# Performance work log

Measured on AMD Instinct MI355X. Metric: run time of the kernel, lower is better.

Reference implementation:

```python
import jax, jax.numpy as jnp
import numpy as np

B, N, M = 8, 4096, 77
Q_DIM, CTX_DIM = 1024, 768
H, D = 16, 64
INNER = H * D  # 1024


def setup_inputs() -> dict:
    key = jax.random.key(0)
    ks = jax.random.split(key, 7)
    x = jax.random.normal(ks[0], (B, N, Q_DIM), dtype=jnp.float32)
    context = jax.random.normal(ks[1], (B, M, CTX_DIM), dtype=jnp.float32)
    # Linear weights stored as [in, out] so y = x @ W (no bias for q/k/v).
    Wq = jax.random.normal(ks[2], (Q_DIM, INNER), dtype=jnp.float32) * (Q_DIM ** -0.5)
    Wk = jax.random.normal(ks[3], (CTX_DIM, INNER), dtype=jnp.float32) * (CTX_DIM ** -0.5)
    Wv = jax.random.normal(ks[4], (CTX_DIM, INNER), dtype=jnp.float32) * (CTX_DIM ** -0.5)
    Wo = jax.random.normal(ks[5], (INNER, Q_DIM), dtype=jnp.float32) * (INNER ** -0.5)
    bo = jax.random.normal(ks[6], (Q_DIM,), dtype=jnp.float32) * 0.01
    return {"x": x, "context": context, "Wq": Wq, "Wk": Wk, "Wv": Wv, "Wo": Wo, "bo": bo}


def reference(x, context, Wq, Wk, Wv, Wo, bo):
    scale = D ** -0.5
    # Project and split heads: [B, S, H*D] -> [B, H, S, D]
    def heads(t):
        b, s, _ = t.shape
        return t.reshape(b, s, H, D).transpose(0, 2, 1, 3)
    q = heads(x @ Wq)        # [B, H, N, D]
    k = heads(context @ Wk)  # [B, H, M, D]
    v = heads(context @ Wv)  # [B, H, M, D]
    scores = jnp.einsum('bhid,bhjd->bhij', q, k) * scale  # [B, H, N, M]
    attn = jax.nn.softmax(scores, axis=-1)
    out = jnp.einsum('bhij,bhjd->bhid', attn, v)          # [B, H, N, D]
    out = out.transpose(0, 2, 1, 3).reshape(x.shape[0], x.shape[1], INNER)
    return out @ Wo + bo  # dropout p=0.0 -> identity
```

## Files before the change

### kernel.cpp

```cpp
#include <hip/hip_runtime.h>
#include <hip/hip_bf16.h>

typedef _Float16 f16x8 __attribute__((ext_vector_type(8)));
typedef float f32x4 __attribute__((ext_vector_type(4)));

#define MFMA16(a, b, c) __builtin_amdgcn_mfma_f32_16x16x32_f16(a, b, c, 0, 0, 0)

__device__ __forceinline__ void load_lds16(const void* g, void* l) {
  __builtin_amdgcn_global_load_lds(
      (__attribute__((address_space(1))) void*)g,
      (__attribute__((address_space(3))) void*)l, 16, 0, 0);
}

__global__ __launch_bounds__(256) void k_cvt16(const float* __restrict__ in,
                                               _Float16* __restrict__ out, int n8) {
  int stride = gridDim.x * blockDim.x;
  for (int i = blockIdx.x * blockDim.x + threadIdx.x; i < n8; i += stride) {
    const float4* p = (const float4*)(in + (size_t)i * 8);
    float4 a = p[0], b = p[1];
    f16x8 v = {(_Float16)a.x, (_Float16)a.y, (_Float16)a.z, (_Float16)a.w,
               (_Float16)b.x, (_Float16)b.y, (_Float16)b.z, (_Float16)b.w};
    *(f16x8*)(out + (size_t)i * 8) = v;
  }
}

__global__ __launch_bounds__(256) void k_transpose(const float* __restrict__ in,
                                                   _Float16* __restrict__ out, int K, int N) {
  __shared__ float tile[64][65];
  int k0 = blockIdx.y * 64, n0 = blockIdx.x * 64;
  int t = threadIdx.x;
  {
    int nn = t & 63, kb = t >> 6;
#pragma unroll
    for (int i = 0; i < 16; ++i) {
      int kk = kb + i * 4;
      tile[kk][nn] = in[(size_t)(k0 + kk) * N + n0 + nn];
    }
  }
  __syncthreads();
  {
    int kk = t & 63, nb = t >> 6;
#pragma unroll
    for (int i = 0; i < 16; ++i) {
      int nn = nb + i * 4;
      out[(size_t)(n0 + nn) * K + k0 + kk] = (_Float16)tile[kk][nn];
    }
  }
}

__global__ __launch_bounds__(64) void k_kvproj(const _Float16* __restrict__ ctxh,
                                               const _Float16* __restrict__ Wkt,
                                               const _Float16* __restrict__ Wvt,
                                               _Float16* __restrict__ Kg,
                                               _Float16* __restrict__ Vtg) {
  int mt = blockIdx.x, nt = blockIdx.y;
  int lane = threadIdx.x;
  int l15 = lane & 15, lhi = lane >> 4;
  int arow = mt * 16 + l15;
  if (arow > 615) arow = 615;
  const _Float16* ap = ctxh + (size_t)arow * 768 + lhi * 8;
  const _Float16* kp = Wkt + (size_t)(nt * 16 + l15) * 768 + lhi * 8;
  const _Float16* vp = Wvt + (size_t)(nt * 16 + l15) * 768 + lhi * 8;
  f32x4 ak = {0.f, 0.f, 0.f, 0.f}, av = {0.f, 0.f, 0.f, 0.f};
#pragma unroll 4
  for (int ks = 0; ks < 24; ++ks) {
    f16x8 a = *(const f16x8*)(ap + ks * 32);
    f16x8 bk = *(const f16x8*)(kp + ks * 32);
    f16x8 bv = *(const f16x8*)(vp + ks * 32);
    ak = MFMA16(a, bk, ak);
    av = MFMA16(a, bv, av);
  }
  int n = nt * 16 + l15, h = n >> 6, d = n & 63;
#pragma unroll
  for (int j = 0; j < 4; ++j) {
    int gm = mt * 16 + lhi * 4 + j;
    if (gm < 616) {
      int b = gm / 77, m = gm - b * 77;
      Kg[((size_t)(b * 16 + h) * 77 + m) * 64 + d] = (_Float16)ak[j];
      Vtg[((size_t)(b * 16 + h) * 64 + d) * 128 + m] = (_Float16)av[j];
    }
  }
}

__global__ __launch_bounds__(256) void k_attn(const _Float16* __restrict__ Qh,
                                              const _Float16* __restrict__ Kg,
                                              const _Float16* __restrict__ Vtg,
                                              _Float16* __restrict__ Out) {
  __shared__ __align__(16) char Kl[80 * 128];
  __shared__ __align__(16) char Vl[64 * 256];
  __shared__ __align__(16) char Pl[4 * 16 * 256];
  int bh = blockIdx.y, b = bh >> 4, h = bh & 15;
  int t = threadIdx.x, wid = t >> 6, lane = t & 63;
  int l15 = lane & 15, lhi = lane >> 4;

  const _Float16* Kgp = Kg + (size_t)bh * (77 * 64);
  const _Float16* Vgp = Vtg + (size_t)bh * (64 * 128);

  for (int idx = t; idx < 640; idx += 256) {
    int m = idx >> 3, c = (idx & 7) * 8;
    f16x8 v = {};
    if (m < 77) v = *(const f16x8*)(Kgp + m * 64 + c);
    *(f16x8*)(Kl + ((m * 128 + c * 2) ^ ((m & 7) << 4))) = v;
  }
  for (int idx = t; idx < 1024; idx += 256) {
    int d = idx >> 4, c = (idx & 15) * 8;
    f16x8 v = *(const f16x8*)(Vgp + d * 128 + c);
    *(f16x8*)(Vl + ((d * 256 + c * 2) ^ ((d & 7) << 4))) = v;
  }
  char* myP = Pl + wid * 4096;
#pragma unroll
  for (int i = 0; i < 4; ++i) *(f16x8*)(myP + lane * 64 + i * 16) = f16x8{};
  __syncthreads();

  int qrow = b * 4096 + blockIdx.x * 64 + wid * 16 + l15;
  const _Float16* qp = Qh + (size_t)qrow * 1024 + h * 64 + lhi * 8;
  f16x8 q0 = *(const f16x8*)qp;
  f16x8 q1 = *(const f16x8*)(qp + 32);

  float e[5][4];
  float mx[4] = {-1e30f, -1e30f, -1e30f, -1e30f};
#pragma unroll
  for (int ct = 0; ct < 5; ++ct) {
    int m = ct * 16 + l15;
    int d0b = lhi * 16;
    f16x8 k0 = *(const f16x8*)(Kl + ((m * 128 + d0b) ^ ((m & 7) << 4)));
    f16x8 k1 = *(const f16x8*)(Kl + ((m * 128 + 64 + d0b) ^ ((m & 7) << 4)));
    f32x4 acc = {0.f, 0.f, 0.f, 0.f};
    acc = MFMA16(q0, k0, acc);
    acc = MFMA16(q1, k1, acc);
    bool valid = m < 77;
#pragma unroll
    for (int j = 0; j < 4; ++j) {
      float v = valid ? acc[j] * 0.125f : -1e30f;
      e[ct][j] = v;
      mx[j] = fmaxf(mx[j], v);
    }
  }
#pragma unroll
  for (int off = 1; off < 16; off <<= 1)
#pragma unroll
    for (int j = 0; j < 4; ++j) mx[j] = fmaxf(mx[j], __shfl_xor(mx[j], off, 64));
  float sm[4] = {0.f, 0.f, 0.f, 0.f};
#pragma unroll
  for (int ct = 0; ct < 5; ++ct)
#pragma unroll
    for (int j = 0; j < 4; ++j) {
      float ev = __expf(e[ct][j] - mx[j]);
      e[ct][j] = ev;
      sm[j] += ev;
    }
#pragma unroll
  for (int off = 1; off < 16; off <<= 1)
#pragma unroll
    for (int j = 0; j < 4; ++j) sm[j] += __shfl_xor(sm[j], off, 64);
  float rs[4];
#pragma unroll
  for (int j = 0; j < 4; ++j) rs[j] = 1.0f / sm[j];

#pragma unroll
  for (int ct = 0; ct < 5; ++ct) {
    int m = ct * 16 + l15;
#pragma unroll
    for (int j = 0; j < 4; ++j) {
      int r = lhi * 4 + j;
      *(_Float16*)(myP + ((r * 256 + m * 2) ^ ((r & 7) << 4))) =
          (_Float16)(e[ct][j] * rs[j]);
    }
  }

  f32x4 o[4] = {{0.f,0.f,0.f,0.f},{0.f,0.f,0.f,0.f},{0.f,0.f,0.f,0.f},{0.f,0.f,0.f,0.f}};
#pragma unroll
  for (int ks = 0; ks < 3; ++ks) {
    int m0b = ks * 64 + lhi * 16;
    f16x8 pa = *(const f16x8*)(myP + ((l15 * 256 + m0b) ^ ((l15 & 7) << 4)));
#pragma unroll
    for (int dt = 0; dt < 4; ++dt) {
      int d = dt * 16 + l15;
      f16x8 vb = *(const f16x8*)(Vl + ((d * 256 + m0b) ^ ((d & 7) << 4)));
      o[dt] = MFMA16(pa, vb, o[dt]);
    }
  }
  _Float16* op = Out + (size_t)(b * 4096 + blockIdx.x * 64 + wid * 16) * 1024 + h * 64;
#pragma unroll
  for (int dt = 0; dt < 4; ++dt)
#pragma unroll
    for (int j = 0; j < 4; ++j) {
      int r = lhi * 4 + j;
      op[(size_t)r * 1024 + dt * 16 + l15] = (_Float16)o[dt][j];
    }
}

template <int FINAL>
__global__ __launch_bounds__(512, 2) void k_gemm3(const _Float16* __restrict__ A,
                                                  const _Float16* __restrict__ Bt,
                                                  void* __restrict__ Cout,
                                                  const float* __restrict__ bias,
                                                  int M, int N, int K) {
  __shared__ __align__(16) char lds[131072];
  const int t = threadIdx.x, wid = t >> 6, lane = t & 63;
  const int wr = wid >> 2, wc = wid & 3;
  const int l15 = lane & 15, lhi = lane >> 4;

  int nwg = gridDim.x, bid = blockIdx.x;
  int wg = ((nwg & 7) == 0) ? ((bid & 7) * (nwg >> 3) + (bid >> 3)) : bid;
  const int nTN = N >> 8;
  const int tm = wg / nTN, tn = wg % nTN;

  const _Float16* Ag = A + (size_t)tm * 256 * K;
  const _Float16* Bg = Bt + (size_t)tn * 256 * K;
  const size_t stg = (size_t)(wid * 8 + (lane >> 3)) * K +
                     (size_t)(((lane & 7) ^ (((lane >> 5) & 1) << 1)) * 8);
  const int dstg = wid * 1024;

  const int xb = ((l15 >> 2) & 1) << 1;
  const int aoff = wr * 16384 + l15 * 128 + ((lhi ^ xb) << 4);
  const int boff = 32768 + wc * 8192 + l15 * 128 + ((lhi ^ xb) << 4);

  f32x4 acc[8][4];
#pragma unroll
  for (int i = 0; i < 8; ++i)
#pragma unroll
    for (int j = 0; j < 4; ++j) acc[i][j] = f32x4{0.f, 0.f, 0.f, 0.f};
  f16x8 a[4][2], b0[2][2], b1[2][2];

#define STG_A(T, RB) load_lds16(Ag + stg + (size_t)(RB) * K + (T) * 64, \
                                lds + ((T) & 1) * 65536 + (RB) * 128 + dstg)
#define STG_B(T, RB) load_lds16(Bg + stg + (size_t)(RB) * K + (T) * 64, \
                                lds + ((T) & 1) * 65536 + 32768 + (RB) * 128 + dstg)
#define RD_A(BUF, MH) { const char* p_ = lds + (BUF) * 65536 + aoff + (MH) * 8192;  \
    _Pragma("unroll") for (int mf = 0; mf < 4; ++mf)                                \
      _Pragma("unroll") for (int kk = 0; kk < 2; ++kk)                              \
        a[mf][kk] = *(const f16x8*)(p_ + mf * 2048 + kk * 64); }
#define RD_B(BUF, NH, BREG) { const char* q_ = lds + (BUF) * 65536 + boff + (NH) * 4096; \
    _Pragma("unroll") for (int nf = 0; nf < 2; ++nf)                                \
      _Pragma("unroll") for (int kk = 0; kk < 2; ++kk)                              \
        BREG[nf][kk] = *(const f16x8*)(q_ + nf * 2048 + kk * 64); }
#define MM(MH, NH, BREG) { __builtin_amdgcn_s_setprio(1);                           \
    _Pragma("unroll") for (int mf = 0; mf < 4; ++mf)                                \
      _Pragma("unroll") for (int nf = 0; nf < 2; ++nf)                              \
        _Pragma("unroll") for (int kk = 0; kk < 2; ++kk)                            \
          acc[(MH)*4+mf][(NH)*2+nf] = MFMA16(a[mf][kk], BREG[nf][kk],               \
                                             acc[(MH)*4+mf][(NH)*2+nf]);            \
    __builtin_amdgcn_s_setprio(0); }
#define VM6 asm volatile("s_waitcnt vmcnt(6)" ::: "memory")
#define VM0 asm volatile("s_waitcnt vmcnt(0)" ::: "memory")
#define BAR __builtin_amdgcn_s_barrier()

  const int nT = K >> 6;

  STG_A(0, 0); STG_A(0, 64); STG_A(0, 128); STG_A(0, 192);
  STG_B(0, 0); STG_B(0, 64); STG_B(0, 128); STG_B(0, 192);
  STG_A(1, 0); STG_A(1, 128);
  STG_B(1, 0); STG_B(1, 64); STG_B(1, 128); STG_B(1, 192);
  asm volatile("s_waitcnt vmcnt(6)" ::: "memory");
  BAR;

  const int nPair = (nT - 2) >> 1;
  for (int i = 0; i < nPair; ++i) {
    const int t0 = 2 * i;
    RD_B(0, 0, b0); RD_A(0, 0); STG_A(t0 + 1, 64); STG_A(t0 + 1, 192); BAR; MM(0, 0, b0); BAR;
    RD_B(0, 1, b1); STG_A(t0 + 2, 0); STG_A(t0 + 2, 128); BAR; MM(0, 1, b1); BAR;
    RD_A(0, 1); STG_B(t0 + 2, 0); STG_B(t0 + 2, 64); BAR; MM(1, 1, b1); BAR;
    STG_B(t0 + 2, 128); STG_B(t0 + 2, 192); VM6; BAR; MM(1, 0, b0); BAR;
    RD_B(1, 0, b0); RD_A(1, 0); STG_A(t0 + 2, 64); STG_A(t0 + 2, 192); BAR; MM(0, 0, b0); BAR;
    RD_B(1, 1, b1); STG_A(t0 + 3, 0); STG_A(t0 + 3, 128); BAR; MM(0, 1, b1); BAR;
    RD_A(1, 1); STG_B(t0 + 3, 0); STG_B(t0 + 3, 64); BAR; MM(1, 1, b1); BAR;
    STG_B(t0 + 3, 128); STG_B(t0 + 3, 192); VM6; BAR; MM(1, 0, b0); BAR;
  }
  RD_B(0, 0, b0); RD_A(0, 0); STG_A(nT - 1, 64); STG_A(nT - 1, 192); BAR; MM(0, 0, b0); BAR;
  RD_B(0, 1, b1); BAR; MM(0, 1, b1); BAR;
  RD_A(0, 1); BAR; MM(1, 1, b1); BAR;
  VM0; BAR; MM(1, 0, b0); BAR;
  RD_B(1, 0, b0); RD_A(1, 0); BAR; MM(0, 0, b0); BAR;
  RD_B(1, 1, b1); BAR; MM(0, 1, b1); BAR;
  RD_A(1, 1); BAR; MM(1, 1, b1); BAR;
  MM(1, 0, b0);

  const long rbase = (long)tm * 256 + wr * 128;
  const int cbase = tn * 256 + wc * 64;
#pragma unroll
  for (int mf = 0; mf < 8; ++mf)
#pragma unroll
    for (int nf = 0; nf < 4; ++nf) {
      int c = cbase + nf * 16 + l15;
      float bv = FINAL ? bias[c] : 0.f;
#pragma unroll
      for (int j = 0; j < 4; ++j) {
        long r = rbase + mf * 16 + lhi * 4 + j;
        float v = acc[mf][nf][j];
        if (FINAL) ((float*)Cout)[r * N + c] = v + bv;
        else ((_Float16*)Cout)[r * N + c] = (_Float16)v;
      }
    }
#undef STG_A
#undef STG_B
#undef RD_A
#undef RD_B
#undef MM
#undef VM6
#undef VM0
#undef BAR
}

extern "C" void kernel_launch(void* const* d_in, const int* in_sizes, int n_in,
                              void* d_out, int out_size, void* d_ws, size_t ws_size,
                              hipStream_t stream) {
  const float* x   = (const float*)d_in[0];
  const float* ctx = (const float*)d_in[1];
  const float* Wq  = (const float*)d_in[2];
  const float* Wk  = (const float*)d_in[3];
  const float* Wv  = (const float*)d_in[4];
  const float* Wo  = (const float*)d_in[5];
  const float* bo  = (const float*)d_in[6];

  char* ws = (char*)d_ws;
  _Float16* xh   = (_Float16*)(ws + 0);
  _Float16* Wqt  = (_Float16*)(ws + 67108864);
  _Float16* Wkt  = (_Float16*)(ws + 69206016);
  _Float16* Wvt  = (_Float16*)(ws + 70778880);
  _Float16* Wot  = (_Float16*)(ws + 72351744);
  _Float16* ctxh = (_Float16*)(ws + 74448896);
  _Float16* Kg   = (_Float16*)(ws + 75395072);
  _Float16* Vtg  = (_Float16*)(ws + 76656640);
  _Float16* Qh   = (_Float16*)d_out;

  k_cvt16<<<4096, 256, 0, stream>>>(x, xh, 33554432 / 8);
  k_cvt16<<<231, 256, 0, stream>>>(ctx, ctxh, 473088 / 8);
  k_transpose<<<dim3(16, 16), 256, 0, stream>>>(Wq, Wqt, 1024, 1024);
  k_transpose<<<dim3(16, 12), 256, 0, stream>>>(Wk, Wkt, 768, 1024);
  k_transpose<<<dim3(16, 12), 256, 0, stream>>>(Wv, Wvt, 768, 1024);
  k_transpose<<<dim3(16, 16), 256, 0, stream>>>(Wo, Wot, 1024, 1024);
  hipMemsetAsync(Vtg, 0, 2097152, stream);
  k_kvproj<<<dim3(39, 64), 64, 0, stream>>>(ctxh, Wkt, Wvt, Kg, Vtg);
  k_gemm3<0><<<dim3(512), dim3(512), 0, stream>>>(xh, Wqt, (void*)Qh, nullptr, 32768, 1024, 1024);
  k_attn<<<dim3(64, 128), 256, 0, stream>>>(Qh, Kg, Vtg, xh);
  k_gemm3<1><<<dim3(512), dim3(512), 0, stream>>>(xh, Wot, d_out, bo, 32768, 1024, 1024);
}
```

Before: 291.9 us.

## Replace 256x256 GEMM with 128x256 tile triple-buffered pipeline

The two large GEMMs (Q projection and output projection) switch from a 256x256 tile with a hand-interleaved double-buffered schedule to a 128x256 tile with a simple three-stage LDS ring, one barrier per K-step, and a full XOR swizzle across 8 chunks. The grid doubles to 1024 workgroups and the accumulator count per thread halves, which gives more waves in flight and fewer barriers per step. In exchange, operand reuse per tile drops, so more global and LDS traffic is needed per FLOP. LDS grows to 144KB per block, which limits each CU to one resident block despite the launch bounds of 2.

```diff
diff --git a/kernel.cpp b/kernel.cpp
--- a/kernel.cpp
+++ b/kernel.cpp
@@ -191,12 +191,12 @@
 }
 
 template <int FINAL>
-__global__ __launch_bounds__(512, 2) void k_gemm3(const _Float16* __restrict__ A,
+__global__ __launch_bounds__(512, 2) void k_gemm4(const _Float16* __restrict__ A,
                                                   const _Float16* __restrict__ Bt,
                                                   void* __restrict__ Cout,
                                                   const float* __restrict__ bias,
                                                   int M, int N, int K) {
-  __shared__ __align__(16) char lds[131072];
+  __shared__ __align__(16) char lds[147456];
   const int t = threadIdx.x, wid = t >> 6, lane = t & 63;
   const int wr = wid >> 2, wc = wid & 3;
   const int l15 = lane & 15, lhi = lane >> 4;
@@ -206,80 +206,77 @@
   const int nTN = N >> 8;
   const int tm = wg / nTN, tn = wg % nTN;
 
-  const _Float16* Ag = A + (size_t)tm * 256 * K;
+  const _Float16* Ag = A + (size_t)tm * 128 * K;
   const _Float16* Bg = Bt + (size_t)tn * 256 * K;
   const size_t stg = (size_t)(wid * 8 + (lane >> 3)) * K +
-                     (size_t)(((lane & 7) ^ (((lane >> 5) & 1) << 1)) * 8);
+                     (size_t)(((lane & 7) ^ ((lane >> 3) & 7)) * 8);
   const int dstg = wid * 1024;
 
-  const int xb = ((l15 >> 2) & 1) << 1;
-  const int aoff = wr * 16384 + l15 * 128 + ((lhi ^ xb) << 4);
-  const int boff = 32768 + wc * 8192 + l15 * 128 + ((lhi ^ xb) << 4);
-
-  f32x4 acc[8][4];
-#pragma unroll
-  for (int i = 0; i < 8; ++i)
+  const int cA = ((lhi ^ (l15 & 7)) << 4);
+
+  f32x4 acc[4][4];
+#pragma unroll
+  for (int i = 0; i < 4; ++i)
 #pragma unroll
     for (int j = 0; j < 4; ++j) acc[i][j] = f32x4{0.f, 0.f, 0.f, 0.f};
-  f16x8 a[4][2], b0[2][2], b1[2][2];
-
-#define STG_A(T, RB) load_lds16(Ag + stg + (size_t)(RB) * K + (T) * 64, \
-                                lds + ((T) & 1) * 65536 + (RB) * 128 + dstg)
-#define STG_B(T, RB) load_lds16(Bg + stg + (size_t)(RB) * K + (T) * 64, \
-                                lds + ((T) & 1) * 65536 + 32768 + (RB) * 128 + dstg)
-#define RD_A(BUF, MH) { const char* p_ = lds + (BUF) * 65536 + aoff + (MH) * 8192;  \
-    _Pragma("unroll") for (int mf = 0; mf < 4; ++mf)                                \
-      _Pragma("unroll") for (int kk = 0; kk < 2; ++kk)                              \
-        a[mf][kk] = *(const f16x8*)(p_ + mf * 2048 + kk * 64); }
-#define RD_B(BUF, NH, BREG) { const char* q_ = lds + (BUF) * 65536 + boff + (NH) * 4096; \
-    _Pragma("unroll") for (int nf = 0; nf < 2; ++nf)                                \
-      _Pragma("unroll") for (int kk = 0; kk < 2; ++kk)                              \
-        BREG[nf][kk] = *(const f16x8*)(q_ + nf * 2048 + kk * 64); }
-#define MM(MH, NH, BREG) { __builtin_amdgcn_s_setprio(1);                           \
-    _Pragma("unroll") for (int mf = 0; mf < 4; ++mf)                                \
-      _Pragma("unroll") for (int nf = 0; nf < 2; ++nf)                              \
-        _Pragma("unroll") for (int kk = 0; kk < 2; ++kk)                            \
-          acc[(MH)*4+mf][(NH)*2+nf] = MFMA16(a[mf][kk], BREG[nf][kk],               \
-                                             acc[(MH)*4+mf][(NH)*2+nf]);            \
-    __builtin_amdgcn_s_setprio(0); }
+
+#define STG_TILE(T, BUF)                                                          \
+  {                                                                               \
+    const size_t co = (size_t)(T) * 64;                                           \
+    char* d = lds + (BUF) * 49152 + dstg;                                         \
+    load_lds16(Ag + stg + co, d);                                                 \
+    load_lds16(Ag + stg + (size_t)64 * K + co, d + 64 * 128);                     \
+    load_lds16(Bg + stg + co, d + 16384);                                         \
+    load_lds16(Bg + stg + (size_t)64 * K + co, d + 16384 + 64 * 128);             \
+    load_lds16(Bg + stg + (size_t)128 * K + co, d + 16384 + 128 * 128);           \
+    load_lds16(Bg + stg + (size_t)192 * K + co, d + 16384 + 192 * 128);           \
+  }
 #define VM6 asm volatile("s_waitcnt vmcnt(6)" ::: "memory")
 #define VM0 asm volatile("s_waitcnt vmcnt(0)" ::: "memory")
 #define BAR __builtin_amdgcn_s_barrier()
 
   const int nT = K >> 6;
 
-  STG_A(0, 0); STG_A(0, 64); STG_A(0, 128); STG_A(0, 192);
-  STG_B(0, 0); STG_B(0, 64); STG_B(0, 128); STG_B(0, 192);
-  STG_A(1, 0); STG_A(1, 128);
-  STG_B(1, 0); STG_B(1, 64); STG_B(1, 128); STG_B(1, 192);
-  asm volatile("s_waitcnt vmcnt(6)" ::: "memory");
-  BAR;
-
-  const int nPair = (nT - 2) >> 1;
-  for (int i = 0; i < nPair; ++i) {
-    const int t0 = 2 * i;
-    RD_B(0, 0, b0); RD_A(0, 0); STG_A(t0 + 1, 64); STG_A(t0 + 1, 192); BAR; MM(0, 0, b0); BAR;
-    RD_B(0, 1, b1); STG_A(t0 + 2, 0); STG_A(t0 + 2, 128); BAR; MM(0, 1, b1); BAR;
-    RD_A(0, 1); STG_B(t0 + 2, 0); STG_B(t0 + 2, 64); BAR; MM(1, 1, b1); BAR;
-    STG_B(t0 + 2, 128); STG_B(t0 + 2, 192); VM6; BAR; MM(1, 0, b0); BAR;
-    RD_B(1, 0, b0); RD_A(1, 0); STG_A(t0 + 2, 64); STG_A(t0 + 2, 192); BAR; MM(0, 0, b0); BAR;
-    RD_B(1, 1, b1); STG_A(t0 + 3, 0); STG_A(t0 + 3, 128); BAR; MM(0, 1, b1); BAR;
-    RD_A(1, 1); STG_B(t0 + 3, 0); STG_B(t0 + 3, 64); BAR; MM(1, 1, b1); BAR;
-    STG_B(t0 + 3, 128); STG_B(t0 + 3, 192); VM6; BAR; MM(1, 0, b0); BAR;
-  }
-  RD_B(0, 0, b0); RD_A(0, 0); STG_A(nT - 1, 64); STG_A(nT - 1, 192); BAR; MM(0, 0, b0); BAR;
-  RD_B(0, 1, b1); BAR; MM(0, 1, b1); BAR;
-  RD_A(0, 1); BAR; MM(1, 1, b1); BAR;
-  VM0; BAR; MM(1, 0, b0); BAR;
-  RD_B(1, 0, b0); RD_A(1, 0); BAR; MM(0, 0, b0); BAR;
-  RD_B(1, 1, b1); BAR; MM(0, 1, b1); BAR;
-  RD_A(1, 1); BAR; MM(1, 1, b1); BAR;
-  MM(1, 0, b0);
-
-  const long rbase = (long)tm * 256 + wr * 128;
+  STG_TILE(0, 0);
+  STG_TILE(1, 1);
+
+  int bufR = 0;
+  for (int tt = 0; tt < nT; ++tt) {
+    if (tt == nT - 1) { VM0; } else { VM6; }
+    BAR;
+    if (tt < nT - 2) {
+      int bufS = bufR + 2; if (bufS >= 3) bufS -= 3;
+      STG_TILE(tt + 2, bufS);
+    }
+    const char* pA = lds + bufR * 49152 + (wr * 64 + l15) * 128 + cA;
+    const char* pB = lds + bufR * 49152 + 16384 + (wc * 64 + l15) * 128 + cA;
+    f16x8 a0[4], a1[4], b0[4], b1[4];
+#pragma unroll
+    for (int mf = 0; mf < 4; ++mf) {
+      a0[mf] = *(const f16x8*)(pA + mf * 2048);
+      a1[mf] = *(const f16x8*)((const char*)((size_t)(pA + mf * 2048) ^ 64));
+    }
+#pragma unroll
+    for (int nf = 0; nf < 4; ++nf) {
+      b0[nf] = *(const f16x8*)(pB + nf * 2048);
+      b1[nf] = *(const f16x8*)((const char*)((size_t)(pB + nf * 2048) ^ 64));
+    }
+    __builtin_amdgcn_s_setprio(1);
+#pragma unroll
+    for (int mf = 0; mf < 4; ++mf)
+#pragma unroll
+      for (int nf = 0; nf < 4; ++nf) {
+        acc[mf][nf] = MFMA16(a0[mf], b0[nf], acc[mf][nf]);
+        acc[mf][nf] = MFMA16(a1[mf], b1[nf], acc[mf][nf]);
+      }
+    __builtin_amdgcn_s_setprio(0);
+    bufR = (bufR == 2) ? 0 : bufR + 1;
+  }
+
+  const long rbase = (long)tm * 128 + wr * 64;
   const int cbase = tn * 256 + wc * 64;
 #pragma unroll
-  for (int mf = 0; mf < 8; ++mf)
+  for (int mf = 0; mf < 4; ++mf)
 #pragma unroll
     for (int nf = 0; nf < 4; ++nf) {
       int c = cbase + nf * 16 + l15;
@@ -292,11 +289,7 @@
         else ((_Float16*)Cout)[r * N + c] = (_Float16)v;
       }
     }
-#undef STG_A
-#undef STG_B
-#undef RD_A
-#undef RD_B
-#undef MM
+#undef STG_TILE
 #undef VM6
 #undef VM0
 #undef BAR
@@ -332,7 +325,7 @@
   k_transpose<<<dim3(16, 16), 256, 0, stream>>>(Wo, Wot, 1024, 1024);
   hipMemsetAsync(Vtg, 0, 2097152, stream);
   k_kvproj<<<dim3(39, 64), 64, 0, stream>>>(ctxh, Wkt, Wvt, Kg, Vtg);
-  k_gemm3<0><<<dim3(512), dim3(512), 0, stream>>>(xh, Wqt, (void*)Qh, nullptr, 32768, 1024, 1024);
+  k_gemm4<0><<<dim3(1024), dim3(512), 0, stream>>>(xh, Wqt, (void*)Qh, nullptr, 32768, 1024, 1024);
   k_attn<<<dim3(64, 128), 256, 0, stream>>>(Qh, Kg, Vtg, xh);
-  k_gemm3<1><<<dim3(512), dim3(512), 0, stream>>>(xh, Wot, d_out, bo, 32768, 1024, 1024);
-}
+  k_gemm4<1><<<dim3(1024), dim3(512), 0, stream>>>(xh, Wot, d_out, bo, 32768, 1024, 1024);
+}
```

After: 320.0 us. +9.6%, slower.
